# Optimization experiments

Measured on AMD Instinct MI355X. Metric: run time of the kernel, lower is better.

Reference implementation:

```python
import jax, jax.numpy as jnp
import numpy as np

B, A, T, NMODE, H = 4, 16, 32, 8, 256
NSCENE = 512
HEADS = 8
FF = 128
LN_EPS = 1e-6

def _layer_norm(x, g, b, eps=LN_EPS):
    mu = jnp.mean(x, axis=-1, keepdims=True)
    var = jnp.mean((x - mu) ** 2, axis=-1, keepdims=True)
    return (x - mu) * jax.lax.rsqrt(var + eps) * g + b


def setup_inputs() -> dict:
    key = jax.random.key(0)
    ks = jax.random.split(key, 16)
    s = 1.0 / np.sqrt(H)
    sf = 1.0 / np.sqrt(FF)
    return {
        "hidden_vecs": jax.random.normal(ks[0], (B, A, T, NMODE, H), jnp.float32),
        "scene_hidden_vec": jax.random.normal(ks[1], (B, NSCENE, H), jnp.float32),
        # nn.MultiheadAttention packed in_proj: rows [Wq; Wk; Wv]
        "in_proj_w": jax.random.normal(ks[2], (3 * H, H), jnp.float32) * s,
        "in_proj_b": jnp.zeros((3 * H,), jnp.float32),
        "out_proj_w": jax.random.normal(ks[3], (H, H), jnp.float32) * s,
        "out_proj_b": jnp.zeros((H,), jnp.float32),
        "attn_ln_g": jnp.ones((H,), jnp.float32),
        "attn_ln_b": jnp.zeros((H,), jnp.float32),
        "ff1_w": jax.random.normal(ks[4], (FF, H), jnp.float32) * s,
        "ff1_b": jnp.zeros((FF,), jnp.float32),
        "ff2_w": jax.random.normal(ks[5], (H, FF), jnp.float32) * sf,
        "ff2_b": jnp.zeros((H,), jnp.float32),
        "ff_ln_g": jnp.ones((H,), jnp.float32),
        "ff_ln_b": jnp.zeros((H,), jnp.float32),
    }


def reference(hidden_vecs, scene_hidden_vec, in_proj_w, in_proj_b, out_proj_w,
              out_proj_b, attn_ln_g, attn_ln_b, ff1_w, ff1_b, ff2_w, ff2_b,
              ff_ln_g, ff_ln_b):
    b, a, t, n, h = hidden_vecs.shape
    N = scene_hidden_vec.shape[1]
    d = h // HEADS
    m = a * t * n  # queries per batch element

    Wq, Wk, Wv = in_proj_w[:h], in_proj_w[h:2 * h], in_proj_w[2 * h:]
    bq, bk, bv = in_proj_b[:h], in_proj_b[h:2 * h], in_proj_b[2 * h:]

    # Project queries; K/V computed ONCE per batch (shared across a,t,n) --
    # avoids materializing the (b,a,t,n,N,h) expanded tensor.
    q = (hidden_vecs.reshape(b, m, h) @ Wq.T + bq).reshape(b, m, HEADS, d)
    k = (scene_hidden_vec @ Wk.T + bk).reshape(b, N, HEADS, d)
    v = (scene_hidden_vec @ Wv.T + bv).reshape(b, N, HEADS, d)

    scale = 1.0 / np.sqrt(d)
    scores = jnp.einsum('bmed,bned->bemn', q * scale, k)  # (b, heads, m, N)
    attn = jax.nn.softmax(scores, axis=-1)
    ctx = jnp.einsum('bemn,bned->bmed', attn, v).reshape(b, m, h)
    attn_out = (ctx @ out_proj_w.T + out_proj_b).reshape(b, a, t, n, h)

    # averaged attention weights over heads (average_attn_weights=True)
    attn_score = jnp.mean(attn, axis=1).reshape(b, a, t, n, 1, N)

    x = _layer_norm(attn_out + hidden_vecs, attn_ln_g, attn_ln_b)
    ff = jax.nn.relu(x @ ff1_w.T + ff1_b) @ ff2_w.T + ff2_b
    out = _layer_norm(ff + x, ff_ln_g, ff_ln_b)
    return out, attn_score
```

## Files before the change

kernel.cpp:

```cpp
#include <hip/hip_runtime.h>
#include <hip/hip_bf16.h>

#define H 256
#define NSC 512
#define MQ 4096
#define BATCH 4

typedef __attribute__((ext_vector_type(8))) short bf16x8;
typedef __attribute__((ext_vector_type(4))) float f32x4;

__device__ __forceinline__ ushort f2bf(float x) {
    union { float f; unsigned u; } c; c.f = x;
    unsigned r = c.u + 0x7FFF + ((c.u >> 16) & 1);
    return (ushort)(r >> 16);
}
__device__ __forceinline__ unsigned pk2(float hi, float lo) {
    union { float f; unsigned u; } a, b; a.f = hi; b.f = lo;
    return __builtin_amdgcn_perm(a.u, b.u, 0x07060302u);
}
__device__ __forceinline__ uint4 cvt8f(const float* p) {
    float4 a = *(const float4*)p;
    float4 b = *(const float4*)(p + 4);
    uint4 r;
    r.x = pk2(a.y, a.x); r.y = pk2(a.w, a.z);
    r.z = pk2(b.y, b.x); r.w = pk2(b.w, b.z);
    return r;
}
#define EXP2(x) __builtin_amdgcn_exp2f(x)

template<int MODE>
__device__ __forceinline__ void gemm_body(
    ushort* As, ushort* Bs, int bx, int by,
    const float* __restrict__ Ain, const float* __restrict__ W,
    const float* __restrict__ bias,
    void* __restrict__ out, ushort* __restrict__ out2,
    int K, int N, float alpha)
{
    const int t = threadIdx.x;
    const int w = t >> 6, lane = t & 63, g = lane >> 4, l15 = lane & 15;
    const int rowBase = by * 64;
    const int colBase = bx * 256;
    const int wr = (w >> 2) * 32;
    const int wc = (w & 3) * 64;
    f32x4 acc[2][4];
    #pragma unroll
    for (int mt = 0; mt < 2; mt++)
        #pragma unroll
        for (int nt = 0; nt < 4; nt++) acc[mt][nt] = (f32x4){0.f,0.f,0.f,0.f};

    const int sr = t >> 3, skc = t & 7, sp = skc ^ (sr & 7);
    const size_t arow = (size_t)(rowBase + sr) * K + skc * 8;

    uint4 av = cvt8f(Ain + arow);
    uint4 bv[4];
    #pragma unroll
    for (int i = 0; i < 4; i++) {
        const int u = t + 512*i, br = u >> 3, bkc = u & 7;
        int brow = colBase + br; if (brow > N - 1) brow = N - 1;
        bv[i] = cvt8f(W + (size_t)brow * K + bkc*8);
    }

    for (int k0 = 0; k0 < K; k0 += 64) {
        __syncthreads();
        *(uint4*)&As[sr*64 + sp*8] = av;
        #pragma unroll
        for (int i = 0; i < 4; i++) {
            const int u = t + 512*i, br = u >> 3, bkc = u & 7, bp = bkc ^ (br & 7);
            *(uint4*)&Bs[br*64 + bp*8] = bv[i];
        }
        __syncthreads();
        if (k0 + 64 < K) {
            av = cvt8f(Ain + arow + k0 + 64);
            #pragma unroll
            for (int i = 0; i < 4; i++) {
                const int u = t + 512*i, br = u >> 3, bkc = u & 7;
                int brow = colBase + br; if (brow > N - 1) brow = N - 1;
                bv[i] = cvt8f(W + (size_t)brow * K + k0 + 64 + bkc*8);
            }
        }
        #pragma unroll
        for (int kk = 0; kk < 2; kk++) {
            const int swz = ((kk*4 + g) ^ (l15 & 7)) * 8;
            bf16x8 af[2], bfr[4];
            #pragma unroll
            for (int mt = 0; mt < 2; mt++)
                af[mt] = *(const bf16x8*)&As[(wr + mt*16 + l15)*64 + swz];
            #pragma unroll
            for (int nt = 0; nt < 4; nt++)
                bfr[nt] = *(const bf16x8*)&Bs[(wc + nt*16 + l15)*64 + swz];
            #pragma unroll
            for (int mt = 0; mt < 2; mt++)
                #pragma unroll
                for (int nt = 0; nt < 4; nt++)
                    acc[mt][nt] = __builtin_amdgcn_mfma_f32_16x16x32_bf16(
                        af[mt], bfr[nt], acc[mt][nt], 0, 0, 0);
        }
    }

    #pragma unroll
    for (int nt = 0; nt < 4; nt++) {
        const int col = colBase + wc + nt*16 + l15;
        const float bb = bias[col];
        #pragma unroll
        for (int mt = 0; mt < 2; mt++) {
            const int row0 = rowBase + wr + mt*16 + g*4;
            if (col < 256) {
                #pragma unroll
                for (int r = 0; r < 4; r++)
                    ((ushort*)out)[(size_t)(row0 + r) * 256 + col] = f2bf(acc[mt][nt][r] + bb);
            } else {
                ushort4 pkv = { f2bf(acc[mt][nt][0] + bb), f2bf(acc[mt][nt][1] + bb),
                                f2bf(acc[mt][nt][2] + bb), f2bf(acc[mt][nt][3] + bb) };
                *(ushort4*)&out2[(size_t)((row0 >> 9)*256 + col - 256) * 512 + (row0 & 511)] = pkv;
            }
        }
    }
}

__global__ __launch_bounds__(512, 4) void kv_kernel(
    const float* __restrict__ scene,
    const float* __restrict__ in_w, const float* __restrict__ in_b,
    ushort* __restrict__ kb, ushort* __restrict__ vtb)
{
    __shared__ ushort As[64 * 64];
    __shared__ ushort Bs[256 * 64];
    gemm_body<1>(As, Bs, blockIdx.x >> 5, blockIdx.x & 31,
                 scene, in_w + 65536, in_b + 256, kb, vtb, 256, 512, 1.f);
}

__global__ __launch_bounds__(1024, 4) void mega_kernel(
    const float* __restrict__ hidden,
    const float* __restrict__ Wq, const float* __restrict__ bq,
    const ushort* __restrict__ k, const ushort* __restrict__ vt,
    const float* __restrict__ Wo, const float* __restrict__ bo,
    const float* __restrict__ ag, const float* __restrict__ ab,
    const float* __restrict__ W1, const float* __restrict__ b1,
    const float* __restrict__ W2, const float* __restrict__ b2,
    const float* __restrict__ fg, const float* __restrict__ fbv,
    float* __restrict__ out, float* __restrict__ attn_score,
    float alpha_q)
{
    __shared__ uint4 SHraw[9120];
    ushort* SH = (ushort*)SHraw;
    ushort* Ks  = SH;
    ushort* Vs  = SH + 8448;
    ushort* Pb  = SH + 18688;
    ushort* As0 = SH;
    ushort* Bs0 = SH + 4096;
    ushort* Bs  = SH;
    ushort* Xb  = SH + 16384;
    float*  Ls  = (float*)(SH + 32768);
    float*  Lq  = (float*)(SH + 33280);
    ushort* Qb  = SH + 39168;
    ushort* Fb  = SH + 39168;
    ushort* Cb  = SH + 55552;
    float*  Lg  = (float*)(SH + 71936);

    const int t = threadIdx.x;
    const int w = t >> 6, lane = t & 63, g = lane >> 4, l15 = lane & 15;
    const int b = blockIdx.x >> 6;
    const int m0 = (blockIdx.x & 63) * 64;
    const size_t rowG = (size_t)b * MQ + m0;
    const size_t kg = (size_t)b * NSC * H;
    const size_t vg = (size_t)b * H * NSC;

    const int wr = (w >> 2) * 16;
    const int wc = (w & 3) * 64;

    {
        f32x4 acc[4];
        #pragma unroll
        for (int nt = 0; nt < 4; nt++) acc[nt] = (f32x4){0.f,0.f,0.f,0.f};

        const int sr = t >> 3, skc = t & 7, sp = skc ^ (sr & 7);
        uint4 av;
        if (t < 512) av = cvt8f(hidden + (rowG + sr) * 256 + skc*8);
        uint4 bv[2];
        #pragma unroll
        for (int i = 0; i < 2; i++) {
            const int u = t + 1024*i, br = u >> 3, bkc = u & 7;
            bv[i] = cvt8f(Wq + (size_t)br * 256 + bkc*8);
        }
        for (int k0 = 0; k0 < 256; k0 += 64) {
            __syncthreads();
            if (t < 512) *(uint4*)&As0[sr*64 + sp*8] = av;
            #pragma unroll
            for (int i = 0; i < 2; i++) {
                const int u = t + 1024*i, br = u >> 3, bkc = u & 7, bp = bkc ^ (br & 7);
                *(uint4*)&Bs0[br*64 + bp*8] = bv[i];
            }
            __syncthreads();
            if (k0 < 192) {
                if (t < 512) av = cvt8f(hidden + (rowG + sr) * 256 + k0 + 64 + skc*8);
                #pragma unroll
                for (int i = 0; i < 2; i++) {
                    const int u = t + 1024*i, br = u >> 3, bkc = u & 7;
                    bv[i] = cvt8f(Wq + (size_t)br * 256 + k0 + 64 + bkc*8);
                }
            }
            #pragma unroll
            for (int kk = 0; kk < 2; kk++) {
                const int swz = ((kk*4 + g) ^ (l15 & 7)) * 8;
                bf16x8 af = *(const bf16x8*)&As0[(wr + l15)*64 + swz];
                #pragma unroll
                for (int nt = 0; nt < 4; nt++) {
                    bf16x8 bfr = *(const bf16x8*)&Bs0[(wc + nt*16 + l15)*64 + swz];
                    acc[nt] = __builtin_amdgcn_mfma_f32_16x16x32_bf16(
                        af, bfr, acc[nt], 0, 0, 0);
                }
            }
        }
        #pragma unroll
        for (int nt = 0; nt < 4; nt++) {
            const int col = wc + nt*16 + l15;
            const float bb = bq[col];
            #pragma unroll
            for (int r = 0; r < 4; r++) {
                const int qr = wr + g*4 + r;
                const float o = (acc[nt][r] + bb) * alpha_q;
                Qb[qr*256 + (((col >> 3) ^ (qr & 7)) << 3) + (col & 7)] = f2bf(o);
            }
        }
    }
    __syncthreads();

    const int hh0 = w & 7, hf = w >> 3;
    bf16x8 qf[2];
    #pragma unroll
    for (int qt = 0; qt < 2; qt++) {
        const int qr0 = hf*32 + qt*16 + l15;
        const int c0 = hh0*32 + g*8;
        qf[qt] = *(const bf16x8*)&Qb[qr0*256 + (((c0 >> 3) ^ (qr0 & 7)) << 3)];
    }

    f32x4 cacc[2][2];
    float lacc[2][4];
    #pragma unroll
    for (int qt = 0; qt < 2; qt++) {
        #pragma unroll
        for (int dt = 0; dt < 2; dt++) cacc[qt][dt] = (f32x4){0.f,0.f,0.f,0.f};
        #pragma unroll
        for (int r = 0; r < 4; r++) lacc[qt][r] = 0.f;
    }

    const int skey = t >> 5, spart = t & 31;
    const int sd = t >> 2, sp2 = t & 3;
    bf16x8 kr = *(const bf16x8*)&k[kg + (size_t)skey*H + spart*8];
    bf16x8 vr = *(const bf16x8*)&vt[vg + (size_t)sd*NSC + sp2*8];

    for (int c = 0; c < 16; c++) {
        const int kbase = c * 32;
        __syncthreads();
        *(bf16x8*)&Ks[skey*264 + spart*8] = kr;
        *(bf16x8*)&Vs[sd*40 + sp2*8] = vr;
        __syncthreads();
        if (c < 15) {
            kr = *(const bf16x8*)&k[kg + (size_t)(kbase + 32 + skey)*H + spart*8];
            vr = *(const bf16x8*)&vt[vg + (size_t)sd*NSC + kbase + 32 + sp2*8];
        }
        #pragma unroll
        for (int qt = 0; qt < 2; qt++) {
            #pragma unroll
            for (int kt = 0; kt < 2; kt++) {
                bf16x8 kf = *(const bf16x8*)&Ks[(kt*16 + l15)*264 + hh0*32 + g*8];
                f32x4 s = __builtin_amdgcn_mfma_f32_16x16x32_bf16(
                    qf[qt], kf, (f32x4){0.f,0.f,0.f,0.f}, 0, 0, 0);
                #pragma unroll
                for (int r = 0; r < 4; r++) {
                    float p = EXP2(s[r]);
                    lacc[qt][r] += p;
                    Pb[(w*32 + qt*16 + g*4 + r)*40 + kt*16 + l15] = f2bf(p);
                }
            }
        }
        #pragma unroll
        for (int qt = 0; qt < 2; qt++) {
            bf16x8 pf = *(const bf16x8*)&Pb[(w*32 + qt*16 + l15)*40 + g*8];
            #pragma unroll
            for (int dt = 0; dt < 2; dt++) {
                bf16x8 vf = *(const bf16x8*)&Vs[(hh0*32 + dt*16 + l15)*40 + g*8];
                cacc[qt][dt] = __builtin_amdgcn_mfma_f32_16x16x32_bf16(
                    pf, vf, cacc[qt][dt], 0, 0, 0);
            }
        }
    }

    #pragma unroll
    for (int qt = 0; qt < 2; qt++) {
        float invl[4];
        #pragma unroll
        for (int r = 0; r < 4; r++) {
            float v = lacc[qt][r];
            v += __shfl_xor(v, 1); v += __shfl_xor(v, 2);
            v += __shfl_xor(v, 4); v += __shfl_xor(v, 8);
            invl[r] = 1.f / v;
            if (l15 == 0) Lg[hh0*64 + hf*32 + qt*16 + g*4 + r] = -__log2f(v) - 3.0f;
        }
        #pragma unroll
        for (int dt = 0; dt < 2; dt++)
            #pragma unroll
            for (int r = 0; r < 4; r++) {
                const int qr = hf*32 + qt*16 + g*4 + r;
                const int col = hh0*32 + dt*16 + l15;
                Cb[qr*256 + (((col >> 3) ^ (qr & 7)) << 3) + (col & 7)]
                    = f2bf(cacc[qt][dt][r] * invl[r]);
            }
    }

    __syncthreads();

    {
        f32x4 sacc[4][2];
        #pragma unroll
        for (int qt = 0; qt < 4; qt++)
            #pragma unroll
            for (int kt = 0; kt < 2; kt++) sacc[qt][kt] = (f32x4){0.f,0.f,0.f,0.f};

        #pragma unroll 2
        for (int h = 0; h < 8; h++) {
            float lgq[4]; bf16x8 qv[4];
            #pragma unroll
            for (int qt = 0; qt < 4; qt++) {
                lgq[qt] = Lg[h*64 + qt*16 + l15];
                const int qr0 = qt*16 + l15;
                const int c0 = h*32 + g*8;
                qv[qt] = *(const bf16x8*)&Qb[qr0*256 + (((c0 >> 3) ^ (qr0 & 7)) << 3)];
            }
            #pragma unroll
            for (int kt = 0; kt < 2; kt++) {
                bf16x8 kf2 = *(const bf16x8*)&k[kg + (size_t)(w*32 + kt*16 + l15)*H + h*32 + g*8];
                #pragma unroll
                for (int qt = 0; qt < 4; qt++) {
                    f32x4 s = __builtin_amdgcn_mfma_f32_16x16x32_bf16(
                        kf2, qv[qt], (f32x4){0.f,0.f,0.f,0.f}, 0, 0, 0);
                    #pragma unroll
                    for (int r = 0; r < 4; r++) sacc[qt][kt][r] += EXP2(s[r] + lgq[qt]);
                }
            }
        }
        #pragma unroll
        for (int qt = 0; qt < 4; qt++)
            #pragma unroll
            for (int kt = 0; kt < 2; kt++)
                *(f32x4*)&attn_score[(rowG + qt*16 + l15)*NSC + w*32 + kt*16 + g*4]
                    = sacc[qt][kt];
    }

    float xres[4][4];
    {
        f32x4 acc[4];
        #pragma unroll
        for (int nt = 0; nt < 4; nt++) acc[nt] = (f32x4){0.f,0.f,0.f,0.f};

        uint4 bv[2];
        #pragma unroll
        for (int i = 0; i < 2; i++) {
            const int u = t + 1024*i, br = u >> 3, bkc = u & 7;
            bv[i] = cvt8f(Wo + (size_t)br * 256 + bkc*8);
        }
        for (int k0 = 0; k0 < 256; k0 += 64) {
            __syncthreads();
            #pragma unroll
            for (int i = 0; i < 2; i++) {
                const int u = t + 1024*i, br = u >> 3, bkc = u & 7, bp = bkc ^ (br & 7);
                *(uint4*)&Bs[br*64 + bp*8] = bv[i];
            }
            __syncthreads();
            if (k0 < 192) {
                #pragma unroll
                for (int i = 0; i < 2; i++) {
                    const int u = t + 1024*i, br = u >> 3, bkc = u & 7;
                    bv[i] = cvt8f(Wo + (size_t)br * 256 + k0 + 64 + bkc*8);
                }
            }
            #pragma unroll
            for (int kk = 0; kk < 2; kk++) {
                const int rowC = wr + l15;
                const int gi = (k0 >> 3) + kk*4 + g;
                bf16x8 af = *(const bf16x8*)&Cb[rowC*256 + ((gi ^ (rowC & 7)) << 3)];
                const int swz = ((kk*4 + g) ^ (l15 & 7)) * 8;
                #pragma unroll
                for (int nt = 0; nt < 4; nt++) {
                    bf16x8 bfr = *(const bf16x8*)&Bs[(wc + nt*16 + l15)*64 + swz];
                    acc[nt] = __builtin_amdgcn_mfma_f32_16x16x32_bf16(
                        af, bfr, acc[nt], 0, 0, 0);
                }
            }
        }
        float bb[4], gmv[4], btv[4];
        #pragma unroll
        for (int nt = 0; nt < 4; nt++) {
            const int col = wc + nt*16 + l15;
            bb[nt] = bo[col]; gmv[nt] = ag[col]; btv[nt] = ab[col];
        }
        #pragma unroll
        for (int r = 0; r < 4; r++) {
            const float* rp = hidden + (rowG + wr + g*4 + r) * 256;
            #pragma unroll
            for (int nt = 0; nt < 4; nt++)
                acc[nt][r] += bb[nt] + rp[wc + nt*16 + l15];
        }
        float ps[4], pq[4];
        #pragma unroll
        for (int r = 0; r < 4; r++) {
            float s = (acc[0][r] + acc[1][r]) + (acc[2][r] + acc[3][r]);
            float qq = (acc[0][r]*acc[0][r] + acc[1][r]*acc[1][r])
                     + (acc[2][r]*acc[2][r] + acc[3][r]*acc[3][r]);
            #pragma unroll
            for (int m = 1; m < 16; m <<= 1) {
                s += __shfl_xor(s, m);
                qq += __shfl_xor(qq, m);
            }
            ps[r] = s; pq[r] = qq;
        }
        if (l15 == 0) {
            #pragma unroll
            for (int r = 0; r < 4; r++) {
                const int ri = wr + g*4 + r;
                Ls[ri*4 + (w & 3)] = ps[r];
                Lq[ri*4 + (w & 3)] = pq[r];
            }
        }
        __syncthreads();
        #pragma unroll
        for (int r = 0; r < 4; r++) {
            const int ri = wr + g*4 + r;
            f32x4 sv = *(const f32x4*)&Ls[ri*4];
            f32x4 qv2 = *(const f32x4*)&Lq[ri*4];
            const float mu = (sv[0]+sv[1]+sv[2]+sv[3]) * (1.f/256.f);
            const float ex2 = (qv2[0]+qv2[1]+qv2[2]+qv2[3]) * (1.f/256.f);
            const float rs = rsqrtf(ex2 - mu*mu + 1e-6f);
            #pragma unroll
            for (int nt = 0; nt < 4; nt++) {
                const int col = wc + nt*16 + l15;
                const float o = (acc[nt][r] - mu) * rs * gmv[nt] + btv[nt];
                xres[nt][r] = o;
                Xb[ri*256 + (((col >> 3) ^ (ri & 7)) << 3) + (col & 7)] = f2bf(o);
            }
        }
    }

    {
        const int wrB = (w >> 2) * 16;
        const int wcB = (w & 3) * 32;
        f32x4 facc[2];
        #pragma unroll
        for (int nt = 0; nt < 2; nt++) facc[nt] = (f32x4){0.f,0.f,0.f,0.f};

        uint4 bv2 = cvt8f(W1 + (size_t)(t >> 3) * 256 + (t & 7)*8);
        for (int k0 = 0; k0 < 256; k0 += 64) {
            __syncthreads();
            {
                const int br = t >> 3, bkc = t & 7, bp = bkc ^ (br & 7);
                *(uint4*)&Bs[br*64 + bp*8] = bv2;
            }
            __syncthreads();
            if (k0 < 192)
                bv2 = cvt8f(W1 + (size_t)(t >> 3) * 256 + k0 + 64 + (t & 7)*8);
            #pragma unroll
            for (int kk = 0; kk < 2; kk++) {
                const int rowX = wrB + l15;
                const int gi = (k0 >> 3) + kk*4 + g;
                bf16x8 af = *(const bf16x8*)&Xb[rowX*256 + ((gi ^ (rowX & 7)) << 3)];
                const int swz = ((kk*4 + g) ^ (l15 & 7)) * 8;
                #pragma unroll
                for (int nt = 0; nt < 2; nt++) {
                    bf16x8 bfr = *(const bf16x8*)&Bs[(wcB + nt*16 + l15)*64 + swz];
                    facc[nt] = __builtin_amdgcn_mfma_f32_16x16x32_bf16(
                        af, bfr, facc[nt], 0, 0, 0);
                }
            }
        }
        __syncthreads();
        #pragma unroll
        for (int nt = 0; nt < 2; nt++) {
            const int colF = wcB + nt*16 + l15;
            const float fbb = b1[colF];
            #pragma unroll
            for (int r = 0; r < 4; r++) {
                const int rowF = wrB + g*4 + r;
                const float o = fmaxf(facc[nt][r] + fbb, 0.f);
                Fb[rowF*128 + (((colF >> 3) ^ (rowF & 7)) << 3) + (colF & 7)] = f2bf(o);
            }
        }
        __syncthreads();
    }

    {
        f32x4 acc2[4];
        #pragma unroll
        for (int nt = 0; nt < 4; nt++) acc2[nt] = (f32x4){0.f,0.f,0.f,0.f};

        uint4 bv3[2];
        #pragma unroll
        for (int i = 0; i < 2; i++) {
            const int u = t + 1024*i, br = u >> 3, bkc = u & 7;
            bv3[i] = cvt8f(W2 + (size_t)br * 128 + bkc*8);
        }
        for (int k0 = 0; k0 < 128; k0 += 64) {
            __syncthreads();
            #pragma unroll
            for (int i = 0; i < 2; i++) {
                const int u = t + 1024*i, br = u >> 3, bkc = u & 7, bp = bkc ^ (br & 7);
                *(uint4*)&Bs[br*64 + bp*8] = bv3[i];
            }
            __syncthreads();
            if (k0 == 0) {
                #pragma unroll
                for (int i = 0; i < 2; i++) {
                    const int u = t + 1024*i, br = u >> 3, bkc = u & 7;
                    bv3[i] = cvt8f(W2 + (size_t)br * 128 + 64 + bkc*8);
                }
            }
            #pragma unroll
            for (int kk = 0; kk < 2; kk++) {
                const int gi = (k0 >> 3) + kk*4 + g;
                const int rowF = wr + l15;
                bf16x8 af2 = *(const bf16x8*)&Fb[rowF*128 + ((gi ^ (rowF & 7)) << 3)];
                const int swz = ((kk*4 + g) ^ (l15 & 7)) * 8;
                #pragma unroll
                for (int nt = 0; nt < 4; nt++) {
                    bf16x8 bfr = *(const bf16x8*)&Bs[(wc + nt*16 + l15)*64 + swz];
                    acc2[nt] = __builtin_amdgcn_mfma_f32_16x16x32_bf16(
                        af2, bfr, acc2[nt], 0, 0, 0);
                }
            }
        }
        float bb[4], gmv[4], btv[4];
        #pragma unroll
        for (int nt = 0; nt < 4; nt++) {
            const int col = wc + nt*16 + l15;
            bb[nt] = b2[col]; gmv[nt] = fg[col]; btv[nt] = fbv[col];
        }
        #pragma unroll
        for (int r = 0; r < 4; r++)
            #pragma unroll
            for (int nt = 0; nt < 4; nt++)
                acc2[nt][r] += bb[nt] + xres[nt][r];
        float ps[4], pq[4];
        #pragma unroll
        for (int r = 0; r < 4; r++) {
            float s = (acc2[0][r] + acc2[1][r]) + (acc2[2][r] + acc2[3][r]);
            float qq = (acc2[0][r]*acc2[0][r] + acc2[1][r]*acc2[1][r])
                     + (acc2[2][r]*acc2[2][r] + acc2[3][r]*acc2[3][r]);
            #pragma unroll
            for (int m = 1; m < 16; m <<= 1) {
                s += __shfl_xor(s, m);
                qq += __shfl_xor(qq, m);
            }
            ps[r] = s; pq[r] = qq;
        }
        __syncthreads();
        if (l15 == 0) {
            #pragma unroll
            for (int r = 0; r < 4; r++) {
                const int ri = wr + g*4 + r;
                Ls[ri*4 + (w & 3)] = ps[r];
                Lq[ri*4 + (w & 3)] = pq[r];
            }
        }
        __syncthreads();
        #pragma unroll
        for (int r = 0; r < 4; r++) {
            const int ri = wr + g*4 + r;
            f32x4 sv = *(const f32x4*)&Ls[ri*4];
            f32x4 qv2 = *(const f32x4*)&Lq[ri*4];
            const float mu = (sv[0]+sv[1]+sv[2]+sv[3]) * (1.f/256.f);
            const float ex2 = (qv2[0]+qv2[1]+qv2[2]+qv2[3]) * (1.f/256.f);
            const float rs = rsqrtf(ex2 - mu*mu + 1e-6f);
            #pragma unroll
            for (int nt = 0; nt < 4; nt++) {
                const int col = wc + nt*16 + l15;
                out[(rowG + ri) * 256 + col] =
                    (acc2[nt][r] - mu) * rs * gmv[nt] + btv[nt];
            }
        }
    }
}

extern "C" void kernel_launch(void* const* d_in, const int* in_sizes, int n_in,
                              void* d_out, int out_size, void* d_ws, size_t ws_size,
                              hipStream_t stream)
{
    const float* hidden = (const float*)d_in[0];
    const float* scene  = (const float*)d_in[1];
    const float* in_w   = (const float*)d_in[2];
    const float* in_b   = (const float*)d_in[3];
    const float* out_w  = (const float*)d_in[4];
    const float* out_b  = (const float*)d_in[5];
    const float* aln_g  = (const float*)d_in[6];
    const float* aln_b  = (const float*)d_in[7];
    const float* ff1_w  = (const float*)d_in[8];
    const float* ff1_b  = (const float*)d_in[9];
    const float* ff2_w  = (const float*)d_in[10];
    const float* ff2_b  = (const float*)d_in[11];
    const float* fln_g  = (const float*)d_in[12];
    const float* fln_b  = (const float*)d_in[13];

    float* out0  = (float*)d_out;
    float* score = out0 + (size_t)BATCH * MQ * H;

    ushort* kb   = (ushort*)d_ws;
    ushort* vtb  = kb + 524288;

    const float alpha_q = 0.25507609683638066f;

    kv_kernel<<<dim3(64), dim3(512), 0, stream>>>(scene, in_w, in_b, kb, vtb);
    mega_kernel<<<dim3(256), dim3(1024), 0, stream>>>(
        hidden, in_w, in_b, kb, vtb,
        out_w, out_b, aln_g, aln_b,
        ff1_w, ff1_b, ff2_w, ff2_b, fln_g, fln_b,
        out0, score, alpha_q);
}
```

Baseline: 167.2 us.

## Fuse KV projection into mega kernel via cooperative grid sync

Folds the K/V projection GEMM into the main kernel. Each of the 256 blocks computes a 16-row by 256-column slice of K/V, then all blocks wait on a cooperative-groups grid barrier before attention starts. This removes the separate kv_kernel launch and its launch gap. In exchange it adds a grid-wide sync and requires a cooperative launch, falling back to the old two-kernel path if that fails. Shared-memory buffers are remapped so the new KV tiles fit alongside the existing ones.

```diff
diff --git a/kernel.cpp b/kernel.cpp
--- a/kernel.cpp
+++ b/kernel.cpp
@@ -1,4 +1,5 @@
 #include <hip/hip_runtime.h>
+#include <hip/hip_cooperative_groups.h>
 #include <hip/hip_bf16.h>
 
 #define H 256
@@ -28,13 +29,11 @@
 }
 #define EXP2(x) __builtin_amdgcn_exp2f(x)
 
-template<int MODE>
-__device__ __forceinline__ void gemm_body(
+__device__ __forceinline__ void gemm_body_kv(
     ushort* As, ushort* Bs, int bx, int by,
     const float* __restrict__ Ain, const float* __restrict__ W,
     const float* __restrict__ bias,
-    void* __restrict__ out, ushort* __restrict__ out2,
-    int K, int N, float alpha)
+    ushort* __restrict__ outk, ushort* __restrict__ out2, int K)
 {
     const int t = threadIdx.x;
     const int w = t >> 6, lane = t & 63, g = lane >> 4, l15 = lane & 15;
@@ -56,8 +55,7 @@
     #pragma unroll
     for (int i = 0; i < 4; i++) {
         const int u = t + 512*i, br = u >> 3, bkc = u & 7;
-        int brow = colBase + br; if (brow > N - 1) brow = N - 1;
-        bv[i] = cvt8f(W + (size_t)brow * K + bkc*8);
+        bv[i] = cvt8f(W + (size_t)(colBase + br) * K + bkc*8);
     }
 
     for (int k0 = 0; k0 < K; k0 += 64) {
@@ -74,8 +72,7 @@
             #pragma unroll
             for (int i = 0; i < 4; i++) {
                 const int u = t + 512*i, br = u >> 3, bkc = u & 7;
-                int brow = colBase + br; if (brow > N - 1) brow = N - 1;
-                bv[i] = cvt8f(W + (size_t)brow * K + k0 + 64 + bkc*8);
+                bv[i] = cvt8f(W + (size_t)(colBase + br) * K + k0 + 64 + bkc*8);
             }
         }
         #pragma unroll
@@ -107,7 +104,7 @@
             if (col < 256) {
                 #pragma unroll
                 for (int r = 0; r < 4; r++)
-                    ((ushort*)out)[(size_t)(row0 + r) * 256 + col] = f2bf(acc[mt][nt][r] + bb);
+                    outk[(size_t)(row0 + r) * 256 + col] = f2bf(acc[mt][nt][r] + bb);
             } else {
                 ushort4 pkv = { f2bf(acc[mt][nt][0] + bb), f2bf(acc[mt][nt][1] + bb),
                                 f2bf(acc[mt][nt][2] + bb), f2bf(acc[mt][nt][3] + bb) };
@@ -124,36 +121,40 @@
 {
     __shared__ ushort As[64 * 64];
     __shared__ ushort Bs[256 * 64];
-    gemm_body<1>(As, Bs, blockIdx.x >> 5, blockIdx.x & 31,
-                 scene, in_w + 65536, in_b + 256, kb, vtb, 256, 512, 1.f);
+    gemm_body_kv(As, Bs, blockIdx.x >> 5, blockIdx.x & 31,
+                 scene, in_w + 65536, in_b + 256, kb, vtb, 256);
 }
 
+namespace cg = cooperative_groups;
+template<int COOP>
 __global__ __launch_bounds__(1024, 4) void mega_kernel(
-    const float* __restrict__ hidden,
-    const float* __restrict__ Wq, const float* __restrict__ bq,
-    const ushort* __restrict__ k, const ushort* __restrict__ vt,
+    const float* __restrict__ hidden, const float* __restrict__ scene,
+    const float* __restrict__ in_w, const float* __restrict__ in_b,
     const float* __restrict__ Wo, const float* __restrict__ bo,
     const float* __restrict__ ag, const float* __restrict__ ab,
     const float* __restrict__ W1, const float* __restrict__ b1,
     const float* __restrict__ W2, const float* __restrict__ b2,
     const float* __restrict__ fg, const float* __restrict__ fbv,
+    ushort* __restrict__ kb, ushort* __restrict__ vtb,
     float* __restrict__ out, float* __restrict__ attn_score,
     float alpha_q)
 {
     __shared__ uint4 SHraw[9120];
     ushort* SH = (ushort*)SHraw;
+    ushort* kvA = SH;
+    ushort* kvB = SH + 1024;
     ushort* Ks  = SH;
     ushort* Vs  = SH + 8448;
     ushort* Pb  = SH + 18688;
     ushort* As0 = SH;
     ushort* Bs0 = SH + 4096;
     ushort* Bs  = SH;
-    ushort* Xb  = SH + 16384;
-    float*  Ls  = (float*)(SH + 32768);
-    float*  Lq  = (float*)(SH + 33280);
+    float*  Ls  = (float*)(SH + 16384);
+    float*  Lq  = (float*)(SH + 16896);
     ushort* Qb  = SH + 39168;
-    ushort* Fb  = SH + 39168;
+    ushort* Xb  = SH + 39168;
     ushort* Cb  = SH + 55552;
+    ushort* Fb  = SH + 55552;
     float*  Lg  = (float*)(SH + 71936);
 
     const int t = threadIdx.x;
@@ -167,6 +168,66 @@
     const int wr = (w >> 2) * 16;
     const int wc = (w & 3) * 64;
 
+    if (COOP) {
+        const int kvt = blockIdx.x >> 2;
+        const int cB  = (kvt >> 5) * 256;
+        const int r0  = (kvt & 31) * 64 + (blockIdx.x & 3) * 16;
+        const float* Wkv = in_w + 65536;
+        const float* bkv = in_b + 256;
+        f32x4 acc = (f32x4){0.f,0.f,0.f,0.f};
+
+        uint4 av;
+        if (t < 128) av = cvt8f(scene + (size_t)(r0 + (t >> 3)) * 256 + (t & 7)*8);
+        uint4 bv[2];
+        #pragma unroll
+        for (int i = 0; i < 2; i++) {
+            const int u = t + 1024*i, br = u >> 3, gi = u & 7;
+            bv[i] = cvt8f(Wkv + (size_t)(cB + br) * 256 + gi*8);
+        }
+        for (int k0 = 0; k0 < 256; k0 += 64) {
+            __syncthreads();
+            if (t < 128) {
+                const int row = t >> 3, gi = t & 7;
+                *(uint4*)&kvA[row*64 + (gi ^ (row & 7))*8] = av;
+            }
+            #pragma unroll
+            for (int i = 0; i < 2; i++) {
+                const int u = t + 1024*i, br = u >> 3, gi = u & 7;
+                *(uint4*)&kvB[br*64 + (gi ^ (br & 7))*8] = bv[i];
+            }
+            __syncthreads();
+            if (k0 < 192) {
+                if (t < 128)
+                    av = cvt8f(scene + (size_t)(r0 + (t >> 3)) * 256 + k0 + 64 + (t & 7)*8);
+                #pragma unroll
+                for (int i = 0; i < 2; i++) {
+                    const int u = t + 1024*i, br = u >> 3, gi = u & 7;
+                    bv[i] = cvt8f(Wkv + (size_t)(cB + br) * 256 + k0 + 64 + gi*8);
+                }
+            }
+            #pragma unroll
+            for (int kk = 0; kk < 2; kk++) {
+                const int swz = ((kk*4 + g) ^ (l15 & 7)) * 8;
+                bf16x8 af = *(const bf16x8*)&kvA[l15*64 + swz];
+                bf16x8 bf = *(const bf16x8*)&kvB[(w*16 + l15)*64 + swz];
+                acc = __builtin_amdgcn_mfma_f32_16x16x32_bf16(af, bf, acc, 0, 0, 0);
+            }
+        }
+        const int col = cB + w*16 + l15;
+        const float bb = bkv[col];
+        if (col < 256) {
+            #pragma unroll
+            for (int r = 0; r < 4; r++)
+                kb[(size_t)(r0 + g*4 + r) * 256 + col] = f2bf(acc[r] + bb);
+        } else {
+            const int row0 = r0 + g*4;
+            ushort4 pkv = { f2bf(acc[0] + bb), f2bf(acc[1] + bb),
+                            f2bf(acc[2] + bb), f2bf(acc[3] + bb) };
+            *(ushort4*)&vtb[(size_t)((row0 >> 9)*256 + col - 256) * 512 + (row0 & 511)] = pkv;
+        }
+        __syncthreads();
+    }
+
     {
         f32x4 acc[4];
         #pragma unroll
@@ -179,7 +240,7 @@
         #pragma unroll
         for (int i = 0; i < 2; i++) {
             const int u = t + 1024*i, br = u >> 3, bkc = u & 7;
-            bv[i] = cvt8f(Wq + (size_t)br * 256 + bkc*8);
+            bv[i] = cvt8f(in_w + (size_t)br * 256 + bkc*8);
         }
         for (int k0 = 0; k0 < 256; k0 += 64) {
             __syncthreads();
@@ -195,7 +256,7 @@
                 #pragma unroll
                 for (int i = 0; i < 2; i++) {
                     const int u = t + 1024*i, br = u >> 3, bkc = u & 7;
-                    bv[i] = cvt8f(Wq + (size_t)br * 256 + k0 + 64 + bkc*8);
+                    bv[i] = cvt8f(in_w + (size_t)br * 256 + k0 + 64 + bkc*8);
                 }
             }
             #pragma unroll
@@ -213,7 +274,7 @@
         #pragma unroll
         for (int nt = 0; nt < 4; nt++) {
             const int col = wc + nt*16 + l15;
-            const float bb = bq[col];
+            const float bb = in_b[col];
             #pragma unroll
             for (int r = 0; r < 4; r++) {
                 const int qr = wr + g*4 + r;
@@ -223,14 +284,18 @@
         }
     }
     __syncthreads();
+
+    if (COOP) {
+        __threadfence();
+        cg::this_grid().sync();
+    }
 
     const int hh0 = w & 7, hf = w >> 3;
     bf16x8 qf[2];
     #pragma unroll
     for (int qt = 0; qt < 2; qt++) {
         const int qr0 = hf*32 + qt*16 + l15;
-        const int c0 = hh0*32 + g*8;
-        qf[qt] = *(const bf16x8*)&Qb[qr0*256 + (((c0 >> 3) ^ (qr0 & 7)) << 3)];
+        qf[qt] = *(const bf16x8*)&Qb[qr0*256 + (((hh0*4 + g) ^ (qr0 & 7)) << 3)];
     }
 
     f32x4 cacc[2][2];
@@ -245,8 +310,8 @@
 
     const int skey = t >> 5, spart = t & 31;
     const int sd = t >> 2, sp2 = t & 3;
-    bf16x8 kr = *(const bf16x8*)&k[kg + (size_t)skey*H + spart*8];
-    bf16x8 vr = *(const bf16x8*)&vt[vg + (size_t)sd*NSC + sp2*8];
+    bf16x8 kr = *(const bf16x8*)&kb[kg + (size_t)skey*H + spart*8];
+    bf16x8 vr = *(const bf16x8*)&vtb[vg + (size_t)sd*NSC + sp2*8];
 
     for (int c = 0; c < 16; c++) {
         const int kbase = c * 32;
@@ -255,8 +320,8 @@
         *(bf16x8*)&Vs[sd*40 + sp2*8] = vr;
         __syncthreads();
         if (c < 15) {
-            kr = *(const bf16x8*)&k[kg + (size_t)(kbase + 32 + skey)*H + spart*8];
-            vr = *(const bf16x8*)&vt[vg + (size_t)sd*NSC + kbase + 32 + sp2*8];
+            kr = *(const bf16x8*)&kb[kg + (size_t)(kbase + 32 + skey)*H + spart*8];
+            vr = *(const bf16x8*)&vtb[vg + (size_t)sd*NSC + kbase + 32 + sp2*8];
         }
         #pragma unroll
         for (int qt = 0; qt < 2; qt++) {
@@ -323,12 +388,11 @@
             for (int qt = 0; qt < 4; qt++) {
                 lgq[qt] = Lg[h*64 + qt*16 + l15];
                 const int qr0 = qt*16 + l15;
-                const int c0 = h*32 + g*8;
-                qv[qt] = *(const bf16x8*)&Qb[qr0*256 + (((c0 >> 3) ^ (qr0 & 7)) << 3)];
+                qv[qt] = *(const bf16x8*)&Qb[qr0*256 + (((h*4 + g) ^ (qr0 & 7)) << 3)];
             }
             #pragma unroll
             for (int kt = 0; kt < 2; kt++) {
-                bf16x8 kf2 = *(const bf16x8*)&k[kg + (size_t)(w*32 + kt*16 + l15)*H + h*32 + g*8];
+                bf16x8 kf2 = *(const bf16x8*)&kb[kg + (size_t)(w*32 + kt*16 + l15)*H + h*32 + g*8];
                 #pragma unroll
                 for (int qt = 0; qt < 4; qt++) {
                     f32x4 s = __builtin_amdgcn_mfma_f32_16x16x32_bf16(
@@ -605,10 +669,34 @@
 
     const float alpha_q = 0.25507609683638066f;
 
-    kv_kernel<<<dim3(64), dim3(512), 0, stream>>>(scene, in_w, in_b, kb, vtb);
-    mega_kernel<<<dim3(256), dim3(1024), 0, stream>>>(
-        hidden, in_w, in_b, kb, vtb,
-        out_w, out_b, aln_g, aln_b,
-        ff1_w, ff1_b, ff2_w, ff2_b, fln_g, fln_b,
-        out0, score, alpha_q);
+    static int coop_ok = -1;
+    if (coop_ok < 0) {
+        int v = 0;
+        hipDeviceGetAttribute(&v, hipDeviceAttributeCooperativeLaunch, 0);
+        coop_ok = v;
+    }
+
+    bool launched = false;
+    if (coop_ok) {
+        void* args[] = {
+            (void*)&hidden, (void*)&scene, (void*)&in_w, (void*)&in_b,
+            (void*)&out_w, (void*)&out_b, (void*)&aln_g, (void*)&aln_b,
+            (void*)&ff1_w, (void*)&ff1_b, (void*)&ff2_w, (void*)&ff2_b,
+            (void*)&fln_g, (void*)&fln_b,
+            (void*)&kb, (void*)&vtb, (void*)&out0, (void*)&score,
+            (void*)&alpha_q
+        };
+        hipError_t e = hipLaunchCooperativeKernel(
+            reinterpret_cast<void*>(&mega_kernel<1>),
+            dim3(256), dim3(1024), args, 0, stream);
+        launched = (e == hipSuccess);
+    }
+    if (!launched) {
+        kv_kernel<<<dim3(64), dim3(512), 0, stream>>>(scene, in_w, in_b, kb, vtb);
+        mega_kernel<0><<<dim3(256), dim3(1024), 0, stream>>>(
+            hidden, scene, in_w, in_b,
+            out_w, out_b, aln_g, aln_b,
+            ff1_w, ff1_b, ff2_w, ff2_b, fln_g, fln_b,
+            kb, vtb, out0, score, alpha_q);
+    }
 }
```

Measured after the change: 271.0 us. 62.1% more time.

## Pre-convert weights to bf16 and fuse attention-score pass into out-proj GEMM

Applied to the files above, without the earlier changes.

The first kernel gets 8 extra blocks that convert Wq, Wo, FF1 and FF2 weights to bf16 once into workspace, so the fused kernel loads bf16 directly instead of converting fp32 per block. The separate head-averaged attention-score loop is interleaved into the out-projection K loop, which overlaps its MFMA/exp work with the GEMM and reuses its loop structure. V fragments are hoisted out of the qt loop, and the shared-memory layout is reshuffled so Xb/Fb alias other buffers. The cost is more register pressure from keeping sacc live across the out-proj GEMM.

```diff
diff --git a/kernel.cpp b/kernel.cpp
--- a/kernel.cpp
+++ b/kernel.cpp
@@ -28,13 +28,11 @@
 }
 #define EXP2(x) __builtin_amdgcn_exp2f(x)
 
-template<int MODE>
-__device__ __forceinline__ void gemm_body(
+__device__ __forceinline__ void gemm_body_kv(
     ushort* As, ushort* Bs, int bx, int by,
     const float* __restrict__ Ain, const float* __restrict__ W,
     const float* __restrict__ bias,
-    void* __restrict__ out, ushort* __restrict__ out2,
-    int K, int N, float alpha)
+    ushort* __restrict__ outk, ushort* __restrict__ out2, int K)
 {
     const int t = threadIdx.x;
     const int w = t >> 6, lane = t & 63, g = lane >> 4, l15 = lane & 15;
@@ -56,8 +54,7 @@
     #pragma unroll
     for (int i = 0; i < 4; i++) {
         const int u = t + 512*i, br = u >> 3, bkc = u & 7;
-        int brow = colBase + br; if (brow > N - 1) brow = N - 1;
-        bv[i] = cvt8f(W + (size_t)brow * K + bkc*8);
+        bv[i] = cvt8f(W + (size_t)(colBase + br) * K + bkc*8);
     }
 
     for (int k0 = 0; k0 < K; k0 += 64) {
@@ -74,8 +71,7 @@
             #pragma unroll
             for (int i = 0; i < 4; i++) {
                 const int u = t + 512*i, br = u >> 3, bkc = u & 7;
-                int brow = colBase + br; if (brow > N - 1) brow = N - 1;
-                bv[i] = cvt8f(W + (size_t)brow * K + k0 + 64 + bkc*8);
+                bv[i] = cvt8f(W + (size_t)(colBase + br) * K + k0 + 64 + bkc*8);
             }
         }
         #pragma unroll
@@ -107,7 +103,7 @@
             if (col < 256) {
                 #pragma unroll
                 for (int r = 0; r < 4; r++)
-                    ((ushort*)out)[(size_t)(row0 + r) * 256 + col] = f2bf(acc[mt][nt][r] + bb);
+                    outk[(size_t)(row0 + r) * 256 + col] = f2bf(acc[mt][nt][r] + bb);
             } else {
                 ushort4 pkv = { f2bf(acc[mt][nt][0] + bb), f2bf(acc[mt][nt][1] + bb),
                                 f2bf(acc[mt][nt][2] + bb), f2bf(acc[mt][nt][3] + bb) };
@@ -120,22 +116,39 @@
 __global__ __launch_bounds__(512, 4) void kv_kernel(
     const float* __restrict__ scene,
     const float* __restrict__ in_w, const float* __restrict__ in_b,
-    ushort* __restrict__ kb, ushort* __restrict__ vtb)
+    const float* __restrict__ out_w, const float* __restrict__ ff1_w,
+    const float* __restrict__ ff2_w,
+    ushort* __restrict__ kb, ushort* __restrict__ vtb,
+    ushort* __restrict__ wsb)
 {
     __shared__ ushort As[64 * 64];
     __shared__ ushort Bs[256 * 64];
-    gemm_body<1>(As, Bs, blockIdx.x >> 5, blockIdx.x & 31,
-                 scene, in_w + 65536, in_b + 256, kb, vtb, 256, 512, 1.f);
+    if (blockIdx.x < 64) {
+        gemm_body_kv(As, Bs, blockIdx.x >> 5, blockIdx.x & 31,
+                     scene, in_w + 65536, in_b + 256, kb, vtb, 256);
+    } else {
+        const int j = blockIdx.x - 64;
+        #pragma unroll
+        for (int i = 0; i < 6; i++) {
+            const int e = j * 24576 + i * 4096 + (int)threadIdx.x * 8;
+            const float* src; int off;
+            if (e < 65536)       { src = in_w;  off = e; }
+            else if (e < 131072) { src = out_w; off = e - 65536; }
+            else if (e < 163840) { src = ff1_w; off = e - 131072; }
+            else                 { src = ff2_w; off = e - 163840; }
+            *(uint4*)&wsb[e] = cvt8f(src + off);
+        }
+    }
 }
 
 __global__ __launch_bounds__(1024, 4) void mega_kernel(
     const float* __restrict__ hidden,
-    const float* __restrict__ Wq, const float* __restrict__ bq,
+    const ushort* __restrict__ Wqb, const float* __restrict__ bq,
     const ushort* __restrict__ k, const ushort* __restrict__ vt,
-    const float* __restrict__ Wo, const float* __restrict__ bo,
+    const ushort* __restrict__ Wob, const float* __restrict__ bo,
     const float* __restrict__ ag, const float* __restrict__ ab,
-    const float* __restrict__ W1, const float* __restrict__ b1,
-    const float* __restrict__ W2, const float* __restrict__ b2,
+    const ushort* __restrict__ W1b, const float* __restrict__ b1,
+    const ushort* __restrict__ W2b, const float* __restrict__ b2,
     const float* __restrict__ fg, const float* __restrict__ fbv,
     float* __restrict__ out, float* __restrict__ attn_score,
     float alpha_q)
@@ -148,12 +161,12 @@
     ushort* As0 = SH;
     ushort* Bs0 = SH + 4096;
     ushort* Bs  = SH;
-    ushort* Xb  = SH + 16384;
-    float*  Ls  = (float*)(SH + 32768);
-    float*  Lq  = (float*)(SH + 33280);
+    float*  Ls  = (float*)(SH + 16384);
+    float*  Lq  = (float*)(SH + 16896);
     ushort* Qb  = SH + 39168;
-    ushort* Fb  = SH + 39168;
+    ushort* Xb  = SH + 39168;
     ushort* Cb  = SH + 55552;
+    ushort* Fb  = SH + 55552;
     float*  Lg  = (float*)(SH + 71936);
 
     const int t = threadIdx.x;
@@ -179,7 +192,7 @@
         #pragma unroll
         for (int i = 0; i < 2; i++) {
             const int u = t + 1024*i, br = u >> 3, bkc = u & 7;
-            bv[i] = cvt8f(Wq + (size_t)br * 256 + bkc*8);
+            bv[i] = *(const uint4*)&Wqb[(size_t)br * 256 + bkc*8];
         }
         for (int k0 = 0; k0 < 256; k0 += 64) {
             __syncthreads();
@@ -195,7 +208,7 @@
                 #pragma unroll
                 for (int i = 0; i < 2; i++) {
                     const int u = t + 1024*i, br = u >> 3, bkc = u & 7;
-                    bv[i] = cvt8f(Wq + (size_t)br * 256 + k0 + 64 + bkc*8);
+                    bv[i] = *(const uint4*)&Wqb[(size_t)br * 256 + k0 + 64 + bkc*8];
                 }
             }
             #pragma unroll
@@ -229,8 +242,7 @@
     #pragma unroll
     for (int qt = 0; qt < 2; qt++) {
         const int qr0 = hf*32 + qt*16 + l15;
-        const int c0 = hh0*32 + g*8;
-        qf[qt] = *(const bf16x8*)&Qb[qr0*256 + (((c0 >> 3) ^ (qr0 & 7)) << 3)];
+        qf[qt] = *(const bf16x8*)&Qb[qr0*256 + (((hh0*4 + g) ^ (qr0 & 7)) << 3)];
     }
 
     f32x4 cacc[2][2];
@@ -258,6 +270,10 @@
             kr = *(const bf16x8*)&k[kg + (size_t)(kbase + 32 + skey)*H + spart*8];
             vr = *(const bf16x8*)&vt[vg + (size_t)sd*NSC + kbase + 32 + sp2*8];
         }
+        bf16x8 vfv[2];
+        #pragma unroll
+        for (int dt = 0; dt < 2; dt++)
+            vfv[dt] = *(const bf16x8*)&Vs[(hh0*32 + dt*16 + l15)*40 + g*8];
         #pragma unroll
         for (int qt = 0; qt < 2; qt++) {
             #pragma unroll
@@ -277,11 +293,9 @@
         for (int qt = 0; qt < 2; qt++) {
             bf16x8 pf = *(const bf16x8*)&Pb[(w*32 + qt*16 + l15)*40 + g*8];
             #pragma unroll
-            for (int dt = 0; dt < 2; dt++) {
-                bf16x8 vf = *(const bf16x8*)&Vs[(hh0*32 + dt*16 + l15)*40 + g*8];
+            for (int dt = 0; dt < 2; dt++)
                 cacc[qt][dt] = __builtin_amdgcn_mfma_f32_16x16x32_bf16(
-                    pf, vf, cacc[qt][dt], 0, 0, 0);
-            }
+                    pf, vfv[dt], cacc[qt][dt], 0, 0, 0);
         }
     }
 
@@ -309,44 +323,12 @@
 
     __syncthreads();
 
-    {
-        f32x4 sacc[4][2];
-        #pragma unroll
-        for (int qt = 0; qt < 4; qt++)
-            #pragma unroll
-            for (int kt = 0; kt < 2; kt++) sacc[qt][kt] = (f32x4){0.f,0.f,0.f,0.f};
-
-        #pragma unroll 2
-        for (int h = 0; h < 8; h++) {
-            float lgq[4]; bf16x8 qv[4];
-            #pragma unroll
-            for (int qt = 0; qt < 4; qt++) {
-                lgq[qt] = Lg[h*64 + qt*16 + l15];
-                const int qr0 = qt*16 + l15;
-                const int c0 = h*32 + g*8;
-                qv[qt] = *(const bf16x8*)&Qb[qr0*256 + (((c0 >> 3) ^ (qr0 & 7)) << 3)];
-            }
-            #pragma unroll
-            for (int kt = 0; kt < 2; kt++) {
-                bf16x8 kf2 = *(const bf16x8*)&k[kg + (size_t)(w*32 + kt*16 + l15)*H + h*32 + g*8];
-                #pragma unroll
-                for (int qt = 0; qt < 4; qt++) {
-                    f32x4 s = __builtin_amdgcn_mfma_f32_16x16x32_bf16(
-                        kf2, qv[qt], (f32x4){0.f,0.f,0.f,0.f}, 0, 0, 0);
-                    #pragma unroll
-                    for (int r = 0; r < 4; r++) sacc[qt][kt][r] += EXP2(s[r] + lgq[qt]);
-                }
-            }
-        }
-        #pragma unroll
-        for (int qt = 0; qt < 4; qt++)
-            #pragma unroll
-            for (int kt = 0; kt < 2; kt++)
-                *(f32x4*)&attn_score[(rowG + qt*16 + l15)*NSC + w*32 + kt*16 + g*4]
-                    = sacc[qt][kt];
-    }
-
     float xres[4][4];
+    f32x4 sacc[4][2];
+    #pragma unroll
+    for (int qt = 0; qt < 4; qt++)
+        #pragma unroll
+        for (int kt = 0; kt < 2; kt++) sacc[qt][kt] = (f32x4){0.f,0.f,0.f,0.f};
     {
         f32x4 acc[4];
         #pragma unroll
@@ -356,7 +338,7 @@
         #pragma unroll
         for (int i = 0; i < 2; i++) {
             const int u = t + 1024*i, br = u >> 3, bkc = u & 7;
-            bv[i] = cvt8f(Wo + (size_t)br * 256 + bkc*8);
+            bv[i] = *(const uint4*)&Wob[(size_t)br * 256 + bkc*8];
         }
         for (int k0 = 0; k0 < 256; k0 += 64) {
             __syncthreads();
@@ -370,7 +352,7 @@
                 #pragma unroll
                 for (int i = 0; i < 2; i++) {
                     const int u = t + 1024*i, br = u >> 3, bkc = u & 7;
-                    bv[i] = cvt8f(Wo + (size_t)br * 256 + k0 + 64 + bkc*8);
+                    bv[i] = *(const uint4*)&Wob[(size_t)br * 256 + k0 + 64 + bkc*8];
                 }
             }
             #pragma unroll
@@ -386,7 +368,36 @@
                         af, bfr, acc[nt], 0, 0, 0);
                 }
             }
-        }
+            #pragma unroll
+            for (int hh = 0; hh < 2; hh++) {
+                const int h = (k0 >> 5) + hh;
+                float lgq[4]; bf16x8 qv[4];
+                #pragma unroll
+                for (int qt = 0; qt < 4; qt++) {
+                    lgq[qt] = Lg[h*64 + qt*16 + l15];
+                    const int qr0 = qt*16 + l15;
+                    qv[qt] = *(const bf16x8*)&Qb[qr0*256 + (((h*4 + g) ^ (qr0 & 7)) << 3)];
+                }
+                #pragma unroll
+                for (int kt = 0; kt < 2; kt++) {
+                    bf16x8 kf2 = *(const bf16x8*)&k[kg + (size_t)(w*32 + kt*16 + l15)*H + h*32 + g*8];
+                    #pragma unroll
+                    for (int qt = 0; qt < 4; qt++) {
+                        f32x4 s = __builtin_amdgcn_mfma_f32_16x16x32_bf16(
+                            kf2, qv[qt], (f32x4){0.f,0.f,0.f,0.f}, 0, 0, 0);
+                        #pragma unroll
+                        for (int r = 0; r < 4; r++) sacc[qt][kt][r] += EXP2(s[r] + lgq[qt]);
+                    }
+                }
+            }
+        }
+        #pragma unroll
+        for (int qt = 0; qt < 4; qt++)
+            #pragma unroll
+            for (int kt = 0; kt < 2; kt++)
+                *(f32x4*)&attn_score[(rowG + qt*16 + l15)*NSC + w*32 + kt*16 + g*4]
+                    = sacc[qt][kt];
+
         float bb[4], gmv[4], btv[4];
         #pragma unroll
         for (int nt = 0; nt < 4; nt++) {
@@ -447,7 +458,7 @@
         #pragma unroll
         for (int nt = 0; nt < 2; nt++) facc[nt] = (f32x4){0.f,0.f,0.f,0.f};
 
-        uint4 bv2 = cvt8f(W1 + (size_t)(t >> 3) * 256 + (t & 7)*8);
+        uint4 bv2 = *(const uint4*)&W1b[(size_t)(t >> 3) * 256 + (t & 7)*8];
         for (int k0 = 0; k0 < 256; k0 += 64) {
             __syncthreads();
             {
@@ -456,7 +467,7 @@
             }
             __syncthreads();
             if (k0 < 192)
-                bv2 = cvt8f(W1 + (size_t)(t >> 3) * 256 + k0 + 64 + (t & 7)*8);
+                bv2 = *(const uint4*)&W1b[(size_t)(t >> 3) * 256 + k0 + 64 + (t & 7)*8];
             #pragma unroll
             for (int kk = 0; kk < 2; kk++) {
                 const int rowX = wrB + l15;
@@ -495,7 +506,7 @@
         #pragma unroll
         for (int i = 0; i < 2; i++) {
             const int u = t + 1024*i, br = u >> 3, bkc = u & 7;
-            bv3[i] = cvt8f(W2 + (size_t)br * 128 + bkc*8);
+            bv3[i] = *(const uint4*)&W2b[(size_t)br * 128 + bkc*8];
         }
         for (int k0 = 0; k0 < 128; k0 += 64) {
             __syncthreads();
@@ -509,7 +520,7 @@
                 #pragma unroll
                 for (int i = 0; i < 2; i++) {
                     const int u = t + 1024*i, br = u >> 3, bkc = u & 7;
-                    bv3[i] = cvt8f(W2 + (size_t)br * 128 + 64 + bkc*8);
+                    bv3[i] = *(const uint4*)&W2b[(size_t)br * 128 + 64 + bkc*8];
                 }
             }
             #pragma unroll
@@ -602,13 +613,15 @@
 
     ushort* kb   = (ushort*)d_ws;
     ushort* vtb  = kb + 524288;
+    ushort* wsb  = vtb + 524288;
 
     const float alpha_q = 0.25507609683638066f;
 
-    kv_kernel<<<dim3(64), dim3(512), 0, stream>>>(scene, in_w, in_b, kb, vtb);
+    kv_kernel<<<dim3(72), dim3(512), 0, stream>>>(
+        scene, in_w, in_b, out_w, ff1_w, ff2_w, kb, vtb, wsb);
     mega_kernel<<<dim3(256), dim3(1024), 0, stream>>>(
-        hidden, in_w, in_b, kb, vtb,
-        out_w, out_b, aln_g, aln_b,
-        ff1_w, ff1_b, ff2_w, ff2_b, fln_g, fln_b,
+        hidden, wsb, in_b, kb, vtb,
+        wsb + 65536, out_b, aln_g, aln_b,
+        wsb + 131072, ff1_b, wsb + 163840, ff2_b, fln_g, fln_b,
         out0, score, alpha_q);
 }
```

Measured after the change: 335.1 us. +100.4%, slower.
